# Kernel optimization log

Hardware: AMD Instinct MI355X
Metric: run time of the kernel (lower is better)

## Reference

```python
import jax, jax.numpy as jnp
import numpy as np

B, T, D_IN, H, C = 4096, 20, 300, 512, 10


def setup_inputs() -> dict:
    key = jax.random.key(0)
    ks = jax.random.split(key, 12)
    s = lambda fan_in, fan_out: float(np.sqrt(6.0 / (fan_in + fan_out)))  # xavier uniform bound
    u = lambda k, shape, b: jax.random.uniform(k, shape, jnp.float32, -b, b)
    return {
        "x": jax.random.normal(ks[0], (B, T, D_IN), jnp.float32),
        "W_emb": u(ks[1], (D_IN, H), s(D_IN, H)),
        "b_emb": jnp.zeros((H,), jnp.float32),
        "wx0": u(ks[2], (H, H), s(H, H)),
        "wh0": u(ks[3], (H, H), s(H, H)),
        "b0": jnp.zeros((H,), jnp.float32),
        "wx1": u(ks[4], (H, H), s(H, H)),
        "wh1": u(ks[5], (H, H), s(H, H)),
        "b1": jnp.zeros((H,), jnp.float32),
        "wx2": u(ks[6], (H, H), s(H, H)),
        "wh2": u(ks[7], (H, H), s(H, H)),
        "b2": jnp.zeros((H,), jnp.float32),
        "W_fc": u(ks[8], (H, C), s(H, C)),
        "b_fc": jnp.zeros((C,), jnp.float32),
    }


def reference(x, W_emb, b_emb, wx0, wh0, b0, wx1, wh1, b1, wx2, wh2, b2, W_fc, b_fc):
    # embedding_layer applied to all timesteps: [B,T,300] -> [B,T,512]
    emb = jnp.einsum("btd,dh->bth", x, W_emb) + b_emb
    h0 = jnp.zeros((x.shape[0], wx0.shape[1]), x.dtype)
    init = (h0, h0, h0)

    def step(carry, v_t):  # v_t: [B,H]
        h0, h1, h2 = carry
        h0 = jnp.tanh(v_t @ wx0 + h0 @ wh0 + b0)
        h1 = jnp.tanh(h0 @ wx1 + h1 @ wh1 + b1)
        h2 = jnp.tanh(h1 @ wx2 + h2 @ wh2 + b2)
        return (h0, h1, h2), None

    (h0, h1, h2), _ = jax.lax.scan(step, init, jnp.swapaxes(emb, 0, 1))  # scan over T
    return h2 @ W_fc + b_fc  # [B, C]
```

## Files before the change

kernel.cpp:

```cpp
#include <hip/hip_runtime.h>

typedef _Float16 f16;
typedef _Float16 f16x8 __attribute__((ext_vector_type(8)));
typedef float floatx4 __attribute__((ext_vector_type(4)));

__device__ __forceinline__ float ftanh(float x) {
  float ax = __builtin_fabsf(x);
  float e  = __expf(-2.0f * ax);
  float t  = (1.0f - e) * __builtin_amdgcn_rcpf(1.0f + e);
  return x < 0.0f ? -t : t;
}

__device__ __forceinline__ void gll16(const f16* g, f16* l) {
  __builtin_amdgcn_global_load_lds(
      (const __attribute__((address_space(1))) void*)g,
      (__attribute__((address_space(3))) void*)l, 16, 0, 0);
}

template<int FJ>
__device__ __forceinline__ void tile_gemm(
    const f16* __restrict__ A0, int ldA0,
    const f16* __restrict__ A1, int ldA1,
    int K, const f16* __restrict__ WT,
    const float* __restrict__ bias,
    f16* __restrict__ outp, int bm, int bn, f16* sm)
{
  const int tid  = threadIdx.x;
  const int w    = tid >> 6;
  const int lane = tid & 63;
  const int lm   = lane & 15;
  const int quad = lane >> 4;
  const int wm   = (w >> 1) * 64;
  const int wn   = (w & 1) * (FJ * 16);
  const int srow8 = lane >> 3;
  const int scol  = ((lane & 7) ^ srow8) * 8;
  const int lmx   = lane & 7;
  constexpr int SB = 8192 + FJ * 2048;

  floatx4 acc[4][FJ];
  #pragma unroll
  for (int i = 0; i < 4; ++i)
    #pragma unroll
    for (int j = 0; j < FJ; ++j)
      acc[i][j] = (floatx4){0.f, 0.f, 0.f, 0.f};

  auto stage = [&](int buf, int k0) {
    const f16* Asrc = (k0 < 512) ? (A0 + k0) : (A1 + (k0 - 512));
    const int  ld   = (k0 < 512) ? ldA0 : ldA1;
    f16* As0 = sm + buf * SB;
    f16* Ws0 = As0 + 8192;
    #pragma unroll
    for (int i = 0; i < 4; ++i) {
      int r = (w * 4 + i) * 8 + srow8;
      gll16(Asrc + (size_t)(bm + r) * ld + scol, As0 + (w * 4 + i) * 512);
    }
    #pragma unroll
    for (int i = 0; i < FJ; ++i) {
      int r = (w * FJ + i) * 8 + srow8;
      gll16(WT + (size_t)(bn + r) * K + k0 + scol, Ws0 + (w * FJ + i) * 512);
    }
  };

  const int NS = K >> 6;
  stage(0, 0);
  __syncthreads();
  for (int s = 0; s < NS; ++s) {
    if (s + 1 < NS) stage((s + 1) & 1, (s + 1) << 6);
    const f16* As0 = sm + (s & 1) * SB;
    const f16* Ws0 = As0 + 8192;
    #pragma unroll
    for (int kk = 0; kk < 64; kk += 32) {
      const int sw = (((kk >> 3) + quad) ^ lmx) << 3;
      f16x8 a[4], bfr[FJ];
      #pragma unroll
      for (int fi = 0; fi < 4; ++fi)
        a[fi] = *(const f16x8*)&As0[(size_t)(wm + fi * 16 + lm) * 64 + sw];
      #pragma unroll
      for (int fj = 0; fj < FJ; ++fj)
        bfr[fj] = *(const f16x8*)&Ws0[(size_t)(wn + fj * 16 + lm) * 64 + sw];
      #pragma unroll
      for (int fi = 0; fi < 4; ++fi)
        #pragma unroll
        for (int fj = 0; fj < FJ; ++fj)
          acc[fi][fj] = __builtin_amdgcn_mfma_f32_16x16x32_f16(a[fi], bfr[fj], acc[fi][fj], 0, 0, 0);
    }
    __syncthreads();
  }

  constexpr int ES = FJ * 32 + 8;
  #pragma unroll
  for (int fi = 0; fi < 4; ++fi)
    #pragma unroll
    for (int fj = 0; fj < FJ; ++fj) {
      int col = wn + fj * 16 + lm;
      #pragma unroll
      for (int r = 0; r < 4; ++r) {
        int row = wm + fi * 16 + quad * 4 + r;
        sm[row * ES + col] = (f16)acc[fi][fj][r];
      }
    }
  __syncthreads();
  constexpr int TPR = (FJ * 32) / 8;
  constexpr int RPP = 256 / TPR;
  #pragma unroll
  for (int p = 0; p < 128 / RPP; ++p) {
    int row = p * RPP + tid / TPR;
    int c8  = (tid % TPR) * 8;
    f16x8 ve = *(const f16x8*)&sm[row * ES + c8];
    floatx4 bv0 = *(const floatx4*)&bias[bn + c8];
    floatx4 bv1 = *(const floatx4*)&bias[bn + c8 + 4];
    union { f16 e[8]; f16x8 v; } o;
    #pragma unroll
    for (int j = 0; j < 4; ++j) o.e[j]     = (f16)ftanh((float)ve[j]     + bv0[j]);
    #pragma unroll
    for (int j = 0; j < 4; ++j) o.e[4 + j] = (f16)ftanh((float)ve[4 + j] + bv1[j]);
    *(f16x8*)(outp + (size_t)(bm + row) * 512 + bn + c8) = o.v;
  }
}

__global__ __launch_bounds__(256, 2)
void rnn_step(int wv, const f16* __restrict__ xh,
              const f16* __restrict__ W0T, const f16* __restrict__ W1T,
              const f16* __restrict__ W2T,
              const float* __restrict__ bcomb, const float* __restrict__ b1,
              const float* __restrict__ b2,
              const f16* __restrict__ H0c, f16* __restrict__ H0n,
              const f16* __restrict__ H1c, f16* __restrict__ H1n,
              const f16* __restrict__ H2c, f16* __restrict__ H2n)
{
  __shared__ f16 sm[32768];
  const int b   = blockIdx.x;
  const int xcd = b & 7;
  const int r   = b >> 3;

  if (r < 32) {
    if (wv > 19) return;
    const int slab = xcd * 4 + (r & 3);
    const int bn   = (r >> 2) * 64;
    tile_gemm<2>(H0c, 512, xh + (size_t)wv * 320, 6400, 832, W0T, bcomb,
                 H0n, slab * 128, bn, sm);
  } else if (r < 48) {
    if (wv < 1 || wv > 20) return;
    const int rr   = r - 32;
    const int slab = xcd * 4 + (rr & 3);
    const int bn   = (rr >> 2) * 128;
    tile_gemm<4>(H0c, 512, H1c, 512, 1024, W1T, b1, H1n, slab * 128, bn, sm);
  } else {
    if (wv < 2) return;
    const int rr   = r - 48;
    const int slab = xcd * 4 + (rr & 3);
    const int bn   = (rr >> 2) * 128;
    tile_gemm<4>(H1c, 512, H2c, 512, 1024, W2T, b2, H2n, slab * 128, bn, sm);
  }
}

#define P_XH  1600
#define P_WCE 4161
#define P_WT  4801
#define P_Z   7873

__global__ __launch_bounds__(256)
void prep_all(const float* __restrict__ x,
              const float* __restrict__ W_emb, const float* __restrict__ b_emb,
              const float* __restrict__ wx0, const float* __restrict__ wh0,
              const float* __restrict__ b0,
              const float* __restrict__ wx1, const float* __restrict__ wh1,
              const float* __restrict__ wx2, const float* __restrict__ wh2,
              f16* __restrict__ xh, f16* __restrict__ W0T,
              f16* __restrict__ W1T, f16* __restrict__ W2T,
              float* __restrict__ bcomb,
              f16* __restrict__ H0a, f16* __restrict__ H1b, f16* __restrict__ H2a)
{
  __shared__ float red[256];
  const int b   = blockIdx.x;
  const int tid = threadIdx.x;

  if (b < P_XH) {
    const int NTH = P_XH * 256;
    const int g = b * 256 + tid;
    floatx4 va[8], vb[8];
    int rw[8], cc[8];
    const floatx4 z4 = {0.f, 0.f, 0.f, 0.f};
    #pragma unroll
    for (int s = 0; s < 8; ++s) {
      int U = g + s * NTH;
      int row = U / 40;
      int c   = (U - row * 40) * 8;
      rw[s] = row; cc[s] = c;
      const float* src = x + (size_t)row * 300 + c;
      va[s] = (c + 4 <= 300) ? *(const floatx4*)src : z4;
      vb[s] = (c + 8 <= 300) ? *(const floatx4*)(src + 4) : z4;
    }
    #pragma unroll
    for (int s = 0; s < 8; ++s) {
      union { f16 e[8]; f16x8 v; } t;
      #pragma unroll
      for (int j = 0; j < 4; ++j) { t.e[j] = (f16)va[s][j]; t.e[4 + j] = (f16)vb[s][j]; }
      *(f16x8*)(xh + (size_t)rw[s] * 320 + cc[s]) = t.v;
    }
  } else if (b < P_WCE) {
    int bb = b - P_XH;
    if (bb < 2560) {
      int oidx  = bb * 64 + (tid & 63);
      int chunk = tid >> 6;
      int n = oidx & 511, k = oidx >> 9;
      float s = 0.f;
      if (k < 300) {
        const float* we = W_emb + k * 512 + chunk * 128;
        const float* wx = wx0 + (size_t)(chunk * 128) * 512 + n;
        #pragma unroll 4
        for (int j = 0; j < 128; ++j)
          s = __builtin_fmaf(we[j], wx[(size_t)j * 512], s);
      }
      red[tid] = s;
      __syncthreads();
      if (chunk == 0)
        W0T[(size_t)n * 832 + 512 + k] =
            (f16)(red[tid] + red[tid + 64] + red[tid + 128] + red[tid + 192]);
    } else {
      #pragma unroll
      for (int p = 0; p < 2; ++p) {
        int n = p * 256 + tid;
        float s = b0[n];
        for (int j = 0; j < 512; ++j)
          s = __builtin_fmaf(b_emb[j], wx0[(size_t)j * 512 + n], s);
        bcomb[n] = s;
      }
    }
  } else if (b < P_WT) {
    int id = (b - P_WCE) * 256 + tid;
    if (id < 32768) {
      int n = id & 511, k8 = id >> 9;
      union { f16 e[8]; f16x8 v; } t;
      #pragma unroll
      for (int j = 0; j < 8; ++j) t.e[j] = (f16)wh0[(size_t)(k8 * 8 + j) * 512 + n];
      *(f16x8*)&W0T[(size_t)n * 832 + k8 * 8] = t.v;
    } else if (id < 98304) {
      int i2 = id - 32768;
      int n = i2 & 511, k8 = i2 >> 9;
      union { f16 e[8]; f16x8 v; } t;
      const float* src = (k8 < 64) ? (wx1 + (size_t)(k8 * 8) * 512 + n)
                                   : (wh1 + (size_t)((k8 - 64) * 8) * 512 + n);
      #pragma unroll
      for (int j = 0; j < 8; ++j) t.e[j] = (f16)src[(size_t)j * 512];
      *(f16x8*)&W1T[(size_t)n * 1024 + k8 * 8] = t.v;
    } else {
      int i2 = id - 98304;
      int n = i2 & 511, k8 = i2 >> 9;
      union { f16 e[8]; f16x8 v; } t;
      const float* src = (k8 < 64) ? (wx2 + (size_t)(k8 * 8) * 512 + n)
                                   : (wh2 + (size_t)((k8 - 64) * 8) * 512 + n);
      #pragma unroll
      for (int j = 0; j < 8; ++j) t.e[j] = (f16)src[(size_t)j * 512];
      *(f16x8*)&W2T[(size_t)n * 1024 + k8 * 8] = t.v;
    }
  } else {
    int id = (b - P_WT) * 256 + tid;
    f16x8 z8 = {};
    f16* dst = (id < 262144) ? H0a : (id < 524288) ? H1b : H2a;
    *(f16x8*)(dst + (size_t)(id & 262143) * 8) = z8;
  }
}

__global__ void fc_kernel(const f16* __restrict__ h2,
                          const float* __restrict__ Wfc, const float* __restrict__ bfc,
                          float* __restrict__ out)
{
  __shared__ float wf[5120];
  __shared__ float bf[16];
  const int tid = threadIdx.x;
  for (int i = tid; i < 5120; i += 256) wf[i] = Wfc[i];
  if (tid < 10) bf[tid] = bfc[tid];
  __syncthreads();
  int id = blockIdx.x * 256 + tid;
  int row = id / 10;
  int c = id - row * 10;
  float s = bf[c];
  const f16* hr = h2 + (size_t)row * 512;
  for (int k8 = 0; k8 < 64; ++k8) {
    f16x8 h8 = *(const f16x8*)(hr + k8 * 8);
    #pragma unroll
    for (int j = 0; j < 8; ++j)
      s = __builtin_fmaf((float)h8[j], wf[(k8 * 8 + j) * 10 + c], s);
  }
  out[id] = s;
}

extern "C" void kernel_launch(void* const* d_in, const int* in_sizes, int n_in,
                              void* d_out, int out_size, void* d_ws, size_t ws_size,
                              hipStream_t stream)
{
  (void)in_sizes; (void)n_in; (void)out_size; (void)ws_size;
  const float* x     = (const float*)d_in[0];
  const float* W_emb = (const float*)d_in[1];
  const float* b_emb = (const float*)d_in[2];
  const float* wx0   = (const float*)d_in[3];
  const float* wh0   = (const float*)d_in[4];
  const float* b0    = (const float*)d_in[5];
  const float* wx1   = (const float*)d_in[6];
  const float* wh1   = (const float*)d_in[7];
  const float* b1    = (const float*)d_in[8];
  const float* wx2   = (const float*)d_in[9];
  const float* wh2   = (const float*)d_in[10];
  const float* b2    = (const float*)d_in[11];
  const float* W_fc  = (const float*)d_in[12];
  const float* b_fc  = (const float*)d_in[13];
  float* out = (float*)d_out;

  char* ws = (char*)d_ws;
  size_t off = 0;
  auto alloc = [&](size_t bytes) -> void* {
    void* p = ws + off;
    off = (off + bytes + 255) & ~(size_t)255;
    return p;
  };
  f16*   xh    = (f16*)alloc((size_t)81920 * 320 * 2);
  f16*   W0T   = (f16*)alloc((size_t)512 * 832 * 2);
  f16*   W1T   = (f16*)alloc((size_t)512 * 1024 * 2);
  f16*   W2T   = (f16*)alloc((size_t)512 * 1024 * 2);
  float* bcomb = (float*)alloc(512 * 4);
  f16*   H0a   = (f16*)alloc((size_t)4096 * 512 * 2);
  f16*   H0b   = (f16*)alloc((size_t)4096 * 512 * 2);
  f16*   H1a   = (f16*)alloc((size_t)4096 * 512 * 2);
  f16*   H1b   = (f16*)alloc((size_t)4096 * 512 * 2);
  f16*   H2a   = (f16*)alloc((size_t)4096 * 512 * 2);
  f16*   H2b   = (f16*)alloc((size_t)4096 * 512 * 2);

  prep_all<<<P_Z, 256, 0, stream>>>(x, W_emb, b_emb, wx0, wh0, b0,
                                    wx1, wh1, wx2, wh2,
                                    xh, W0T, W1T, W2T, bcomb, H0a, H1b, H2a);

  for (int wv = 0; wv < 22; ++wv) {
    const int cur = wv & 1;
    f16* H0c = cur ? H0b : H0a;  f16* H0n = cur ? H0a : H0b;
    f16* H1c = cur ? H1b : H1a;  f16* H1n = cur ? H1a : H1b;
    f16* H2c = cur ? H2b : H2a;  f16* H2n = cur ? H2a : H2b;
    rnn_step<<<512, 256, 0, stream>>>(wv, xh, W0T, W1T, W2T, bcomb, b1, b2,
                                      H0c, H0n, H1c, H1n, H2c, H2n);
  }

  fc_kernel<<<160, 256, 0, stream>>>(H2a, W_fc, b_fc, out);
}
```

Baseline: 592.1 us.

## Use 8 waves per GEMM tile and parallelize bias-combine prep

The recurrent step kernel now launches 512-thread blocks, eight waves per block, with each wave covering a 32-row slice instead of 64. The same tile shape gets more waves to hide load and MFMA latency, at the cost of less operand reuse per wave. The prep kernel is split into an x-conversion kernel and a weight kernel. The combined bias, which was a serial 512-step loop in one block, is now computed by 8 blocks with a shared-memory reduction to remove that tail.

```diff
diff --git a/kernel.cpp b/kernel.cpp
--- a/kernel.cpp
+++ b/kernel.cpp
@@ -25,23 +25,25 @@
     const float* __restrict__ bias,
     f16* __restrict__ outp, int bm, int bn, f16* sm)
 {
+  constexpr int TN = FJ * 32;
+  constexpr int NJ = FJ;
   const int tid  = threadIdx.x;
   const int w    = tid >> 6;
   const int lane = tid & 63;
   const int lm   = lane & 15;
   const int quad = lane >> 4;
-  const int wm   = (w >> 1) * 64;
-  const int wn   = (w & 1) * (FJ * 16);
+  const int wm   = (w >> 1) * 32;
+  const int wn   = (w & 1) * (TN / 2);
   const int srow8 = lane >> 3;
   const int scol  = ((lane & 7) ^ srow8) * 8;
   const int lmx   = lane & 7;
-  constexpr int SB = 8192 + FJ * 2048;
-
-  floatx4 acc[4][FJ];
-  #pragma unroll
-  for (int i = 0; i < 4; ++i)
-    #pragma unroll
-    for (int j = 0; j < FJ; ++j)
+  constexpr int SB = 8192 + TN * 64;
+
+  floatx4 acc[2][NJ];
+  #pragma unroll
+  for (int i = 0; i < 2; ++i)
+    #pragma unroll
+    for (int j = 0; j < NJ; ++j)
       acc[i][j] = (floatx4){0.f, 0.f, 0.f, 0.f};
 
   auto stage = [&](int buf, int k0) {
@@ -50,14 +52,14 @@
     f16* As0 = sm + buf * SB;
     f16* Ws0 = As0 + 8192;
     #pragma unroll
-    for (int i = 0; i < 4; ++i) {
-      int r = (w * 4 + i) * 8 + srow8;
-      gll16(Asrc + (size_t)(bm + r) * ld + scol, As0 + (w * 4 + i) * 512);
-    }
-    #pragma unroll
-    for (int i = 0; i < FJ; ++i) {
-      int r = (w * FJ + i) * 8 + srow8;
-      gll16(WT + (size_t)(bn + r) * K + k0 + scol, Ws0 + (w * FJ + i) * 512);
+    for (int i = 0; i < 2; ++i) {
+      int r = w * 16 + i * 8 + srow8;
+      gll16(Asrc + (size_t)(bm + r) * ld + scol, As0 + (w * 2 + i) * 512);
+    }
+    #pragma unroll
+    for (int i = 0; i < TN / 64; ++i) {
+      int r = (w * (TN / 64) + i) * 8 + srow8;
+      gll16(WT + (size_t)(bn + r) * K + k0 + scol, Ws0 + (w * (TN / 64) + i) * 512);
     }
   };
 
@@ -71,37 +73,37 @@
     #pragma unroll
     for (int kk = 0; kk < 64; kk += 32) {
       const int sw = (((kk >> 3) + quad) ^ lmx) << 3;
-      f16x8 a[4], bfr[FJ];
-      #pragma unroll
-      for (int fi = 0; fi < 4; ++fi)
-        a[fi] = *(const f16x8*)&As0[(size_t)(wm + fi * 16 + lm) * 64 + sw];
-      #pragma unroll
-      for (int fj = 0; fj < FJ; ++fj)
-        bfr[fj] = *(const f16x8*)&Ws0[(size_t)(wn + fj * 16 + lm) * 64 + sw];
-      #pragma unroll
-      for (int fi = 0; fi < 4; ++fi)
+      f16x8 a[2], bfr[NJ];
+      #pragma unroll
+      for (int mi = 0; mi < 2; ++mi)
+        a[mi] = *(const f16x8*)&As0[(size_t)(wm + mi * 16 + lm) * 64 + sw];
+      #pragma unroll
+      for (int nj = 0; nj < NJ; ++nj)
+        bfr[nj] = *(const f16x8*)&Ws0[(size_t)(wn + nj * 16 + lm) * 64 + sw];
+      #pragma unroll
+      for (int mi = 0; mi < 2; ++mi)
         #pragma unroll
-        for (int fj = 0; fj < FJ; ++fj)
-          acc[fi][fj] = __builtin_amdgcn_mfma_f32_16x16x32_f16(a[fi], bfr[fj], acc[fi][fj], 0, 0, 0);
+        for (int nj = 0; nj < NJ; ++nj)
+          acc[mi][nj] = __builtin_amdgcn_mfma_f32_16x16x32_f16(a[mi], bfr[nj], acc[mi][nj], 0, 0, 0);
     }
     __syncthreads();
   }
 
-  constexpr int ES = FJ * 32 + 8;
-  #pragma unroll
-  for (int fi = 0; fi < 4; ++fi)
-    #pragma unroll
-    for (int fj = 0; fj < FJ; ++fj) {
-      int col = wn + fj * 16 + lm;
+  constexpr int ES = TN + 8;
+  #pragma unroll
+  for (int mi = 0; mi < 2; ++mi)
+    #pragma unroll
+    for (int nj = 0; nj < NJ; ++nj) {
+      int col = wn + nj * 16 + lm;
       #pragma unroll
       for (int r = 0; r < 4; ++r) {
-        int row = wm + fi * 16 + quad * 4 + r;
-        sm[row * ES + col] = (f16)acc[fi][fj][r];
+        int row = wm + mi * 16 + quad * 4 + r;
+        sm[row * ES + col] = (f16)acc[mi][nj][r];
       }
     }
   __syncthreads();
-  constexpr int TPR = (FJ * 32) / 8;
-  constexpr int RPP = 256 / TPR;
+  constexpr int TPR = TN / 8;
+  constexpr int RPP = 512 / TPR;
   #pragma unroll
   for (int p = 0; p < 128 / RPP; ++p) {
     int row = p * RPP + tid / TPR;
@@ -118,7 +120,7 @@
   }
 }
 
-__global__ __launch_bounds__(256, 2)
+__global__ __launch_bounds__(512, 4)
 void rnn_step(int wv, const f16* __restrict__ xh,
               const f16* __restrict__ W0T, const f16* __restrict__ W1T,
               const f16* __restrict__ W2T,
@@ -154,81 +156,86 @@
   }
 }
 
-#define P_XH  1600
-#define P_WCE 4161
-#define P_WT  4801
-#define P_Z   7873
+#define PX_N 1600
 
 __global__ __launch_bounds__(256)
-void prep_all(const float* __restrict__ x,
-              const float* __restrict__ W_emb, const float* __restrict__ b_emb,
-              const float* __restrict__ wx0, const float* __restrict__ wh0,
-              const float* __restrict__ b0,
-              const float* __restrict__ wx1, const float* __restrict__ wh1,
-              const float* __restrict__ wx2, const float* __restrict__ wh2,
-              f16* __restrict__ xh, f16* __restrict__ W0T,
-              f16* __restrict__ W1T, f16* __restrict__ W2T,
-              float* __restrict__ bcomb,
-              f16* __restrict__ H0a, f16* __restrict__ H1b, f16* __restrict__ H2a)
+void prep_x(const float* __restrict__ x, f16* __restrict__ xh)
+{
+  const int NTH = PX_N * 256;
+  const int g = blockIdx.x * 256 + threadIdx.x;
+  floatx4 va[8], vb[8];
+  int rw[8], cc[8];
+  const floatx4 z4 = {0.f, 0.f, 0.f, 0.f};
+  #pragma unroll
+  for (int s = 0; s < 8; ++s) {
+    int U = g + s * NTH;
+    int row = U / 40;
+    int c   = (U - row * 40) * 8;
+    rw[s] = row; cc[s] = c;
+    const float* src = x + (size_t)row * 300 + c;
+    va[s] = (c + 4 <= 300) ? *(const floatx4*)src : z4;
+    vb[s] = (c + 8 <= 300) ? *(const floatx4*)(src + 4) : z4;
+  }
+  #pragma unroll
+  for (int s = 0; s < 8; ++s) {
+    union { f16 e[8]; f16x8 v; } t;
+    #pragma unroll
+    for (int j = 0; j < 4; ++j) { t.e[j] = (f16)va[s][j]; t.e[4 + j] = (f16)vb[s][j]; }
+    *(f16x8*)(xh + (size_t)rw[s] * 320 + cc[s]) = t.v;
+  }
+}
+
+#define PW_WCE 2560
+#define PW_BC  2568
+#define PW_WT  3208
+#define PW_Z   6280
+
+__global__ __launch_bounds__(256)
+void prep_w(const float* __restrict__ W_emb, const float* __restrict__ b_emb,
+            const float* __restrict__ wx0, const float* __restrict__ wh0,
+            const float* __restrict__ b0,
+            const float* __restrict__ wx1, const float* __restrict__ wh1,
+            const float* __restrict__ wx2, const float* __restrict__ wh2,
+            f16* __restrict__ W0T, f16* __restrict__ W1T, f16* __restrict__ W2T,
+            float* __restrict__ bcomb,
+            f16* __restrict__ H0a, f16* __restrict__ H1b, f16* __restrict__ H2a)
 {
   __shared__ float red[256];
   const int b   = blockIdx.x;
   const int tid = threadIdx.x;
 
-  if (b < P_XH) {
-    const int NTH = P_XH * 256;
-    const int g = b * 256 + tid;
-    floatx4 va[8], vb[8];
-    int rw[8], cc[8];
-    const floatx4 z4 = {0.f, 0.f, 0.f, 0.f};
-    #pragma unroll
-    for (int s = 0; s < 8; ++s) {
-      int U = g + s * NTH;
-      int row = U / 40;
-      int c   = (U - row * 40) * 8;
-      rw[s] = row; cc[s] = c;
-      const float* src = x + (size_t)row * 300 + c;
-      va[s] = (c + 4 <= 300) ? *(const floatx4*)src : z4;
-      vb[s] = (c + 8 <= 300) ? *(const floatx4*)(src + 4) : z4;
-    }
-    #pragma unroll
-    for (int s = 0; s < 8; ++s) {
-      union { f16 e[8]; f16x8 v; } t;
-      #pragma unroll
-      for (int j = 0; j < 4; ++j) { t.e[j] = (f16)va[s][j]; t.e[4 + j] = (f16)vb[s][j]; }
-      *(f16x8*)(xh + (size_t)rw[s] * 320 + cc[s]) = t.v;
-    }
-  } else if (b < P_WCE) {
-    int bb = b - P_XH;
-    if (bb < 2560) {
-      int oidx  = bb * 64 + (tid & 63);
-      int chunk = tid >> 6;
-      int n = oidx & 511, k = oidx >> 9;
-      float s = 0.f;
-      if (k < 300) {
-        const float* we = W_emb + k * 512 + chunk * 128;
-        const float* wx = wx0 + (size_t)(chunk * 128) * 512 + n;
-        #pragma unroll 4
-        for (int j = 0; j < 128; ++j)
-          s = __builtin_fmaf(we[j], wx[(size_t)j * 512], s);
-      }
-      red[tid] = s;
-      __syncthreads();
-      if (chunk == 0)
-        W0T[(size_t)n * 832 + 512 + k] =
-            (f16)(red[tid] + red[tid + 64] + red[tid + 128] + red[tid + 192]);
-    } else {
-      #pragma unroll
-      for (int p = 0; p < 2; ++p) {
-        int n = p * 256 + tid;
-        float s = b0[n];
-        for (int j = 0; j < 512; ++j)
-          s = __builtin_fmaf(b_emb[j], wx0[(size_t)j * 512 + n], s);
-        bcomb[n] = s;
-      }
-    }
-  } else if (b < P_WT) {
-    int id = (b - P_WCE) * 256 + tid;
+  if (b < PW_WCE) {
+    int oidx  = b * 64 + (tid & 63);
+    int chunk = tid >> 6;
+    int n = oidx & 511, k = oidx >> 9;
+    float s = 0.f;
+    if (k < 300) {
+      const float* we = W_emb + k * 512 + chunk * 128;
+      const float* wx = wx0 + (size_t)(chunk * 128) * 512 + n;
+      #pragma unroll 4
+      for (int j = 0; j < 128; ++j)
+        s = __builtin_fmaf(we[j], wx[(size_t)j * 512], s);
+    }
+    red[tid] = s;
+    __syncthreads();
+    if (chunk == 0)
+      W0T[(size_t)n * 832 + 512 + k] =
+          (f16)(red[tid] + red[tid + 64] + red[tid + 128] + red[tid + 192]);
+  } else if (b < PW_BC) {
+    int n     = (b - PW_WCE) * 64 + (tid & 63);
+    int chunk = tid >> 6;
+    float s = 0.f;
+    const float* be = b_emb + chunk * 128;
+    const float* wx = wx0 + (size_t)(chunk * 128) * 512 + n;
+    #pragma unroll 4
+    for (int j = 0; j < 128; ++j)
+      s = __builtin_fmaf(be[j], wx[(size_t)j * 512], s);
+    red[tid] = s;
+    __syncthreads();
+    if (chunk == 0)
+      bcomb[n] = b0[n] + red[tid] + red[tid + 64] + red[tid + 128] + red[tid + 192];
+  } else if (b < PW_WT) {
+    int id = (b - PW_BC) * 256 + tid;
     if (id < 32768) {
       int n = id & 511, k8 = id >> 9;
       union { f16 e[8]; f16x8 v; } t;
@@ -255,7 +262,7 @@
       *(f16x8*)&W2T[(size_t)n * 1024 + k8 * 8] = t.v;
     }
   } else {
-    int id = (b - P_WT) * 256 + tid;
+    int id = (b - PW_WT) * 256 + tid;
     f16x8 z8 = {};
     f16* dst = (id < 262144) ? H0a : (id < 524288) ? H1b : H2a;
     *(f16x8*)(dst + (size_t)(id & 262143) * 8) = z8;
@@ -326,16 +333,17 @@
   f16*   H2a   = (f16*)alloc((size_t)4096 * 512 * 2);
   f16*   H2b   = (f16*)alloc((size_t)4096 * 512 * 2);
 
-  prep_all<<<P_Z, 256, 0, stream>>>(x, W_emb, b_emb, wx0, wh0, b0,
-                                    wx1, wh1, wx2, wh2,
-                                    xh, W0T, W1T, W2T, bcomb, H0a, H1b, H2a);
+  prep_x<<<PX_N, 256, 0, stream>>>(x, xh);
+  prep_w<<<PW_Z, 256, 0, stream>>>(W_emb, b_emb, wx0, wh0, b0,
+                                   wx1, wh1, wx2, wh2,
+                                   W0T, W1T, W2T, bcomb, H0a, H1b, H2a);
 
   for (int wv = 0; wv < 22; ++wv) {
     const int cur = wv & 1;
     f16* H0c = cur ? H0b : H0a;  f16* H0n = cur ? H0a : H0b;
     f16* H1c = cur ? H1b : H1a;  f16* H1n = cur ? H1a : H1b;
     f16* H2c = cur ? H2b : H2a;  f16* H2n = cur ? H2a : H2b;
-    rnn_step<<<512, 256, 0, stream>>>(wv, xh, W0T, W1T, W2T, bcomb, b1, b2,
+    rnn_step<<<512, 512, 0, stream>>>(wv, xh, W0T, W1T, W2T, bcomb, b1, b2,
                                       H0c, H0n, H1c, H1n, H2c, H2n);
   }
 
```

After: 596.0 us. No clear change (+0.7%).
